# Kernel tuning notes

Measured on AMD Instinct MI355X. Metric: run time of the kernel, lower is better.

The kernel has to match this reference:

```python
import jax, jax.numpy as jnp
import numpy as np

DIM, DIN, NST, RK, K, BATCH, H, W = 64, 128, 16, 4, 4, 1, 128, 128


def conv2d(x, w, b=None, pad=0, groups=1):
    y = jax.lax.conv_general_dilated(x, w, (1, 1), [(pad, pad), (pad, pad)],
                                     dimension_numbers=('NCHW', 'OIHW', 'NCHW'),
                                     feature_group_count=groups)
    return y if b is None else y + b[None, :, None, None]


def layer_norm(x, g, b, eps=1e-5):
    mu = x.mean(-1, keepdims=True)
    var = x.var(-1, keepdims=True)
    return (x - mu) * jax.lax.rsqrt(var + eps) * g + b


def selective_scan(u, delta, A, Bs, Cs, D):
    # u, delta: (B,K,Din,L); A: (K,Din,N); Bs,Cs: (B,K,N,L); D: (K,Din)
    uT = jnp.moveaxis(u, -1, 0)
    dT = jnp.moveaxis(delta, -1, 0)
    BT = jnp.moveaxis(Bs, -1, 0)
    CT = jnp.moveaxis(Cs, -1, 0)
    h0 = jnp.zeros(u.shape[:3] + (A.shape[-1],), u.dtype)

    def step(h, inp):
        u_t, d_t, B_t, C_t = inp
        h = h * jnp.exp(d_t[..., None] * A) + (d_t * u_t)[..., None] * B_t[:, :, None, :]
        return h, jnp.einsum('bkdn,bkn->bkd', h, C_t)

    _, ys = jax.lax.scan(step, h0, (uT, dT, BT, CT))
    return jnp.moveaxis(ys, 0, -1) + u * D[None, :, :, None]


def ss2d(x, in_proj_w, conv_dw_w, conv_dw_b, x_proj_w, dt_w, dt_b, A_logs, Ds, on_g, on_b, out_w):
    # x: (B,H,W,C) -- VMamba-style SS2D with 4 scan directions
    Bb, Hh, Ww, C = x.shape
    L = Hh * Ww
    xz = jnp.einsum('bhwc,ec->bhwe', x, in_proj_w)
    xa, z = jnp.split(xz, 2, axis=-1)
    xa = jax.nn.silu(conv2d(xa.transpose(0, 3, 1, 2), conv_dw_w, conv_dw_b, pad=1, groups=DIN))
    x0 = xa.reshape(Bb, DIN, L)                          # row-major scan
    x1 = xa.transpose(0, 1, 3, 2).reshape(Bb, DIN, L)    # column-major scan
    xs = jnp.stack([x0, x1, jnp.flip(x0, -1), jnp.flip(x1, -1)], axis=1)  # (B,4,Din,L)
    x_dbl = jnp.einsum('bkdl,kcd->bkcl', xs, x_proj_w)
    dts, Bs, Cs = x_dbl[:, :, :RK], x_dbl[:, :, RK:RK + NST], x_dbl[:, :, RK + NST:]
    delta = jax.nn.softplus(jnp.einsum('bkrl,kdr->bkdl', dts, dt_w) + dt_b[None, :, :, None])
    ys = selective_scan(xs, delta, -jnp.exp(A_logs), Bs, Cs, Ds)  # (B,4,Din,L)

    def unwh(t):
        return t.reshape(Bb, DIN, Ww, Hh).transpose(0, 1, 3, 2).reshape(Bb, DIN, L)

    y = ys[:, 0] + jnp.flip(ys[:, 2], -1) + unwh(ys[:, 1]) + unwh(jnp.flip(ys[:, 3], -1))
    y = layer_norm(y.transpose(0, 2, 1).reshape(Bb, Hh, Ww, DIN), on_g, on_b)
    return jnp.einsum('bhwd,cd->bhwc', y * jax.nn.silu(z), out_w)


def setup_inputs():
    key = jax.random.key(0)
    ks = jax.random.split(key, 24)
    n = lambda k, s, sc=0.05: jax.random.normal(k, s, jnp.float32) * sc
    return dict(
        x=n(ks[0], (BATCH, DIM, H, W), 1.0),
        conv1_w=n(ks[1], (DIM, DIM, 3, 3)), conv1_b=n(ks[2], (DIM,)),
        conv2_w=n(ks[3], (DIM, DIM, 5, 5)), conv2_b=n(ks[4], (DIM,)),
        dw1a_w=n(ks[5], (2 * DIM, 2, 3, 3)), dw1a_b=n(ks[6], (2 * DIM,)),
        dw1b_w=n(ks[7], (DIM, 2 * DIM, 1, 1)), dw1b_b=n(ks[8], (DIM,)),
        dw2a_w=n(ks[9], (DIM, 1, 3, 3)), dw2a_b=n(ks[10], (DIM,)),
        dw2b_w=n(ks[11], (DIM, DIM, 1, 1)), dw2b_b=n(ks[12], (DIM,)),
        ln_g=jnp.ones((DIM,), jnp.float32), ln_b=jnp.zeros((DIM,), jnp.float32),
        in_proj_w=n(ks[13], (2 * DIN, DIM)),
        conv_dw_w=n(ks[14], (DIN, 1, 3, 3)), conv_dw_b=n(ks[15], (DIN,)),
        x_proj_w=n(ks[16], (K, RK + 2 * NST, DIN)),
        dt_w=n(ks[17], (K, DIN, RK)), dt_b=jnp.full((K, DIN), 0.01, jnp.float32),
        A_logs=jnp.tile(jnp.log(jnp.arange(1, NST + 1, dtype=jnp.float32)), (K, DIN, 1)),
        Ds=jnp.ones((K, DIN), jnp.float32),
        on_g=jnp.ones((DIN,), jnp.float32), on_b=jnp.zeros((DIN,), jnp.float32),
        out_w=n(ks[18], (DIM, DIN)),
    )


def reference(x, conv1_w, conv1_b, conv2_w, conv2_b, dw1a_w, dw1a_b, dw1b_w, dw1b_b,
              dw2a_w, dw2a_b, dw2b_w, dw2b_b, ln_g, ln_b, in_proj_w, conv_dw_w, conv_dw_b,
              x_proj_w, dt_w, dt_b, A_logs, Ds, on_g, on_b, out_w):
    res = x
    y = jax.nn.relu(jnp.concatenate([conv2d(x, conv1_w, conv1_b, pad=1),
                                     conv2d(x, conv2_w, conv2_b, pad=2)], axis=1))
    y = jax.nn.relu(conv2d(conv2d(y, dw1a_w, dw1a_b, pad=1, groups=DIM), dw1b_w, dw1b_b))
    # F.layer_norm over (C,H,W), no affine
    mu = y.mean((1, 2, 3), keepdims=True)
    var = y.var((1, 2, 3), keepdims=True)
    y = (y - mu) * jax.lax.rsqrt(var + 1e-5)
    # SS2D block: pre-LN + SS2D + residual, in NHWC
    yp = y.transpose(0, 2, 3, 1)
    yp = yp + ss2d(layer_norm(yp, ln_g, ln_b), in_proj_w, conv_dw_w, conv_dw_b,
                   x_proj_w, dt_w, dt_b, A_logs, Ds, on_g, on_b, out_w)
    y = yp.transpose(0, 3, 1, 2)
    y = jax.nn.relu(conv2d(conv2d(y, dw2a_w, dw2a_b, pad=1, groups=DIM), dw2b_w, dw2b_b))
    return y + res
```

## Files before the change

kernel.cpp:

```cpp
#include <hip/hip_runtime.h>

#define L 16384
#define NCH 128
#define CT  128

__device__ __forceinline__ float softplusf(float x){
  return (x > 20.f) ? x : log1pf(__expf(x));
}
__device__ __forceinline__ float siluf(float x){
  return x / (1.f + __expf(-x));
}
__device__ __forceinline__ float wave_sum(float v){
  #pragma unroll
  for (int o = 32; o; o >>= 1) v += __shfl_xor(v, o);
  return v;
}

__global__ __launch_bounds__(256) void k_prep(
    const float* __restrict__ w1, const float* __restrict__ w2,
    const float* __restrict__ ipw,
    float* __restrict__ wT1, float* __restrict__ wT2, float* __restrict__ ipwT)
{
  int g = blockIdx.x * 256 + threadIdx.x;
  if (g < 36864){
    int ci = g / 576, rem = g % 576, co = rem / 9, tap = rem % 9;
    wT1[g] = w1[(co*64 + ci)*9 + tap];
  } else if (g < 36864 + 102400){
    int g2 = g - 36864;
    int ci = g2 / 1600, rem = g2 % 1600, co = rem / 25, tap = rem % 25;
    wT2[g2] = w2[(co*64 + ci)*25 + tap];
  } else if (g < 36864 + 102400 + 16384){
    int g3 = g - 139264;
    int e = g3 & 255, c = g3 >> 8;
    ipwT[g3] = ipw[e*64 + c];
  }
}

template<int KS>
__global__ __launch_bounds__(256) void k_convC(
    const float* __restrict__ x, const float* __restrict__ wT,
    const float* __restrict__ b, float* __restrict__ y)
{
  constexpr int P = KS/2, NT = KS*KS;
  const int tid = threadIdx.x;
  const int col = tid & 127;
  const int rh  = tid >> 7;
  const int cg  = blockIdx.x & 15;
  const int rq  = blockIdx.x >> 4;
  const int r0  = rq*4 + rh*2;
  const int co0 = cg*4;
  float acc[2][4];
  #pragma unroll
  for (int a = 0; a < 4; ++a){ acc[0][a] = b[co0+a]; acc[1][a] = acc[0][a]; }

  for (int ci = 0; ci < 64; ++ci){
    const float* xp = x + ci*L;
    const float* wp = wT + (ci*64 + co0)*NT;
    #pragma unroll
    for (int ir = 0; ir < KS+1; ++ir){
      int gr = r0 - P + ir;
      float xrow[KS];
      if ((unsigned)gr < 128u){
        const float* xr = xp + gr*128;
        #pragma unroll
        for (int kx = 0; kx < KS; ++kx){
          int cc = col + kx - P;
          xrow[kx] = ((unsigned)cc < 128u) ? xr[cc] : 0.f;
        }
      } else {
        #pragma unroll
        for (int kx = 0; kx < KS; ++kx) xrow[kx] = 0.f;
      }
      #pragma unroll
      for (int q = 0; q < 2; ++q){
        int ky = ir - q;
        if (ky >= 0 && ky < KS){
          #pragma unroll
          for (int kx = 0; kx < KS; ++kx){
            #pragma unroll
            for (int a = 0; a < 4; ++a)
              acc[q][a] = fmaf(xrow[kx], wp[a*NT + ky*KS + kx], acc[q][a]);
          }
        }
      }
    }
  }
  #pragma unroll
  for (int q = 0; q < 2; ++q){
    const int p = (r0+q)*128 + col;
    #pragma unroll
    for (int a = 0; a < 4; ++a)
      y[(co0+a)*L + p] = fmaxf(acc[q][a], 0.f);
  }
}

__global__ __launch_bounds__(256) void k_dw1a(
    const float* __restrict__ y1, const float* __restrict__ w, const float* __restrict__ b,
    float* __restrict__ t1)
{
  int g = blockIdx.x * 256 + threadIdx.x;
  int p = g & (L-1);
  int o = g >> 14;
  int h = p >> 7, ww = p & 127;
  int grp = o >> 1;
  float acc = b[o];
  #pragma unroll
  for (int i = 0; i < 2; ++i){
    const float* xp = y1 + (grp*2 + i)*L;
    const float* wp = w + (o*2 + i)*9;
    #pragma unroll
    for (int ky = 0; ky < 3; ++ky){
      int hh = h + ky - 1;
      if ((unsigned)hh < 128u){
        #pragma unroll
        for (int kx = 0; kx < 3; ++kx){
          int wx = ww + kx - 1;
          if ((unsigned)wx < 128u)
            acc = fmaf(xp[hh*128 + wx], wp[ky*3+kx], acc);
        }
      }
    }
  }
  t1[o*L + p] = acc;
}

__global__ __launch_bounds__(256) void k_dw1b(
    const float* __restrict__ t1, const float* __restrict__ w, const float* __restrict__ b,
    float* __restrict__ y2, float* __restrict__ red)
{
  __shared__ float s[16][130];
  __shared__ float rs[4][2];
  int p0 = blockIdx.x * 16;
  for (int i = threadIdx.x; i < 2048; i += 256){
    int ci = i >> 4, dp = i & 15;
    s[dp][ci] = t1[ci*L + p0 + dp];
  }
  __syncthreads();
  int dp = threadIdx.x & 15, cg = threadIdx.x >> 4;
  float lsum = 0.f, lsq = 0.f;
  #pragma unroll
  for (int cc = 0; cc < 4; ++cc){
    int c = cg + cc*16;
    float acc = b[c];
    const float* wp = w + c*128;
    #pragma unroll 8
    for (int i = 0; i < 128; ++i) acc = fmaf(s[dp][i], wp[i], acc);
    acc = fmaxf(acc, 0.f);
    y2[c*L + p0 + dp] = acc;
    lsum += acc; lsq += acc*acc;
  }
  lsum = wave_sum(lsum); lsq = wave_sum(lsq);
  if ((threadIdx.x & 63) == 0){ rs[threadIdx.x>>6][0] = lsum; rs[threadIdx.x>>6][1] = lsq; }
  __syncthreads();
  if (threadIdx.x == 0){
    float a = rs[0][0]+rs[1][0]+rs[2][0]+rs[3][0];
    float q = rs[0][1]+rs[1][1]+rs[2][1]+rs[3][1];
    atomicAdd(&red[0], a);
    atomicAdd(&red[1], q);
  }
}

__global__ __launch_bounds__(256) void k_norm_inproj(
    const float* __restrict__ y2, const float* __restrict__ red,
    const float* __restrict__ ln_g, const float* __restrict__ ln_b,
    const float* __restrict__ ipwT,
    float* __restrict__ ynorm, float* __restrict__ xa_pre, float* __restrict__ sz)
{
  __shared__ float ws_s[16384];
  __shared__ float ls_s[64*33];
  __shared__ float mv_s[2][32];
  const int tid = threadIdx.x;
  const int p0 = blockIdx.x * 32;
  {
    const float4* src = (const float4*)ipwT;
    float4* dst = (float4*)ws_s;
    #pragma unroll
    for (int i = 0; i < 16; ++i) dst[tid + i*256] = src[tid + i*256];
  }
  const float invN = 1.f / 1048576.f;
  float mu = red[0] * invN;
  float var = red[1] * invN - mu*mu;
  float rsg = rsqrtf(var + 1e-5f);
  for (int i = tid; i < 2048; i += 256){
    int c = i >> 5, pix = i & 31;
    ls_s[c*33 + pix] = (y2[c*L + p0 + pix] - mu) * rsg;
  }
  __syncthreads();
  for (int i = tid; i < 2048; i += 256){
    int pix = i >> 6, c = i & 63;
    ynorm[(p0 + pix)*64 + c] = ls_s[c*33 + pix];
  }
  if (tid < 32){
    float s = 0.f, q = 0.f;
    #pragma unroll 8
    for (int c = 0; c < 64; ++c){
      float v = ls_s[c*33 + tid];
      s += v; q += v*v;
    }
    float m = s * (1.f/64.f);
    float va = q * (1.f/64.f) - m*m;
    mv_s[0][tid] = m;
    mv_s[1][tid] = rsqrtf(va + 1e-5f);
  }
  __syncthreads();
  for (int i = tid; i < 2048; i += 256){
    int c = i >> 5, pix = i & 31;
    float v = ls_s[c*33 + pix];
    ls_s[c*33 + pix] = (v - mv_s[0][pix]) * mv_s[1][pix] * ln_g[c] + ln_b[c];
  }
  __syncthreads();
  const int pix = tid & 31, eh = tid >> 5;
  float acc[32];
  #pragma unroll
  for (int j = 0; j < 32; ++j) acc[j] = 0.f;
  for (int c = 0; c < 64; ++c){
    float lnv = ls_s[c*33 + pix];
    const float4* w4 = (const float4*)(ws_s + c*256 + eh*32);
    #pragma unroll
    for (int j = 0; j < 8; ++j){
      float4 wq = w4[j];
      acc[j*4+0] = fmaf(lnv, wq.x, acc[j*4+0]);
      acc[j*4+1] = fmaf(lnv, wq.y, acc[j*4+1]);
      acc[j*4+2] = fmaf(lnv, wq.z, acc[j*4+2]);
      acc[j*4+3] = fmaf(lnv, wq.w, acc[j*4+3]);
    }
  }
  __syncthreads();
  float* szs = ws_s;
  const int p = p0 + pix;
  if (eh < 4){
    const int e0 = eh*32;
    #pragma unroll
    for (int j = 0; j < 32; ++j)
      xa_pre[(e0+j)*L + p] = acc[j];
  } else {
    const int j0 = (eh-4)*32;
    #pragma unroll
    for (int j = 0; j < 32; ++j)
      szs[pix*129 + j0 + j] = siluf(acc[j]);
  }
  __syncthreads();
  for (int i = tid; i < 32*128; i += 256){
    int pix2 = i >> 7, j = i & 127;
    sz[(p0 + pix2)*128 + j] = szs[pix2*129 + j];
  }
}

__global__ __launch_bounds__(256) void k_dwc(
    const float* __restrict__ xa, const float* __restrict__ w, const float* __restrict__ b,
    float* __restrict__ u)
{
  int g = blockIdx.x * 256 + threadIdx.x;
  int p = g & (L-1);
  int d = g >> 14;
  int h = p >> 7, ww = p & 127;
  const float* xp = xa + d*L;
  const float* wp = w + d*9;
  float acc = b[d];
  #pragma unroll
  for (int ky = 0; ky < 3; ++ky){
    int hh = h + ky - 1;
    if ((unsigned)hh < 128u){
      #pragma unroll
      for (int kx = 0; kx < 3; ++kx){
        int wx = ww + kx - 1;
        if ((unsigned)wx < 128u)
          acc = fmaf(xp[hh*128 + wx], wp[ky*3+kx], acc);
      }
    }
  }
  u[d*L + p] = siluf(acc);
}

template<int PASS>
__global__ __launch_bounds__(256) void k_proj(
    const float* __restrict__ u, const float* __restrict__ xw,
    const float* __restrict__ dtw, const float* __restrict__ dtb,
    float* __restrict__ delta_s, float* __restrict__ Bs, float* __restrict__ Cs,
    float* __restrict__ u_out)
{
  __shared__ float us[16][132];
  __shared__ float dts[16][2][4];
  int bb = blockIdx.x;
  int tid = threadIdx.x;
  for (int i = tid; i < 16*128; i += 256){
    int d = i >> 4, pix = i & 15;
    int idx = bb*16 + pix;
    int p;
    if (PASS == 0) p = idx;
    else           p = (idx & 127)*128 + (idx >> 7);
    us[pix][d] = u[d*L + p];
  }
  __syncthreads();
  for (int o = tid; o < 1152; o += 256){
    int pix = o / 72; int r = o % 72; int kk = r / 36; int c = r % 36;
    int k = (PASS == 0) ? kk*2 : kk*2 + 1;
    const float4* ur = (const float4*)(&us[pix][0]);
    const float4* wr = (const float4*)(xw + (k*36 + c)*128);
    float acc = 0.f;
    #pragma unroll
    for (int i = 0; i < 32; ++i){
      float4 a = ur[i], bw = wr[i];
      acc = fmaf(a.x, bw.x, acc); acc = fmaf(a.y, bw.y, acc);
      acc = fmaf(a.z, bw.z, acc); acc = fmaf(a.w, bw.w, acc);
    }
    int idx = bb*16 + pix;
    if (c < 4)        dts[pix][kk][c] = acc;
    else if (c < 20)  Bs[(k*L + idx)*16 + (c-4)]  = acc;
    else              Cs[(k*L + idx)*16 + (c-20)] = acc;
  }
  __syncthreads();
  int d = tid & 127, ph = tid >> 7;
  #pragma unroll
  for (int pp = 0; pp < 8; ++pp){
    int pix = pp*2 + ph;
    int idx = bb*16 + pix;
    #pragma unroll
    for (int kk = 0; kk < 2; ++kk){
      int k = (PASS == 0) ? kk*2 : kk*2 + 1;
      const float4 dw = *((const float4*)(dtw + (k*128 + d)*4));
      float acc = dtb[k*128 + d];
      acc = fmaf(dts[pix][kk][0], dw.x, acc);
      acc = fmaf(dts[pix][kk][1], dw.y, acc);
      acc = fmaf(dts[pix][kk][2], dw.z, acc);
      acc = fmaf(dts[pix][kk][3], dw.w, acc);
      delta_s[(k*L + idx)*128 + d] = softplusf(acc);
    }
    u_out[idx*128 + d] = us[pix][d];
  }
}

__global__ __launch_bounds__(256) void k_scan1(
    const float* __restrict__ delta_s, const float* __restrict__ u_row,
    const float* __restrict__ u_col, const float* __restrict__ Bs,
    const float* __restrict__ Alog, float* __restrict__ P, float* __restrict__ S)
{
  int blk = blockIdx.x;
  int k = blk >> 7, ch = blk & (NCH-1);
  int tid = threadIdx.x;
  int d = tid & 127, nh = tid >> 7;
  const float* u_s = (k & 1) ? u_col : u_row;
  float A[8], Pv[8], Sv[8];
  #pragma unroll
  for (int j = 0; j < 8; ++j){
    A[j] = -__expf(Alog[(k*128 + d)*16 + nh*8 + j]);
    Pv[j] = 1.f; Sv[j] = 0.f;
  }
  int base = ch*CT;
  for (int t = 0; t < CT; ++t){
    int tl = base + t;
    int pos = (k < 2) ? tl : (L-1 - tl);
    float dl = delta_s[(k*L + pos)*128 + d];
    float du = dl * u_s[pos*128 + d];
    const float* Br = Bs + (k*L + pos)*16 + nh*8;
    #pragma unroll
    for (int j = 0; j < 8; ++j){
      float a = __expf(dl * A[j]);
      Sv[j] = fmaf(Sv[j], a, du * Br[j]);
      Pv[j] *= a;
    }
  }
  #pragma unroll
  for (int j = 0; j < 8; ++j){
    int o = (blk*16 + nh*8 + j)*128 + d;
    P[o] = Pv[j]; S[o] = Sv[j];
  }
}

__global__ __launch_bounds__(256) void k_scan2(
    const float* __restrict__ P, const float* __restrict__ S, float* __restrict__ hst)
{
  int g = blockIdx.x * 256 + threadIdx.x;
  int d = g & 127, n = (g >> 7) & 15, k = g >> 11;
  float h = 0.f;
  for (int c = 0; c < NCH; ++c){
    int o = (((k*NCH + c)*16) + n)*128 + d;
    hst[o] = h;
    h = fmaf(P[o], h, S[o]);
  }
}

__global__ __launch_bounds__(256) void k_scan3(
    const float* __restrict__ delta_s, const float* __restrict__ u_row,
    const float* __restrict__ u_col, const float* __restrict__ Bs,
    const float* __restrict__ Cs, const float* __restrict__ Alog,
    const float* __restrict__ hst, float* __restrict__ ys)
{
  int blk = blockIdx.x;
  int k = blk >> 7, ch = blk & (NCH-1);
  int tid = threadIdx.x;
  int d = tid >> 1, nh = tid & 1;
  const float* u_s = (k & 1) ? u_col : u_row;
  float A[8], h[8];
  #pragma unroll
  for (int j = 0; j < 8; ++j){
    A[j] = -__expf(Alog[(k*128 + d)*16 + nh*8 + j]);
    h[j] = hst[(blk*16 + nh*8 + j)*128 + d];
  }
  int base = ch*CT;
  for (int t = 0; t < CT; ++t){
    int tl = base + t;
    int pos = (k < 2) ? tl : (L-1 - tl);
    float dl = delta_s[(k*L + pos)*128 + d];
    float du = dl * u_s[pos*128 + d];
    const float* Br = Bs + (k*L + pos)*16 + nh*8;
    const float* Cr = Cs + (k*L + pos)*16 + nh*8;
    float y = 0.f;
    #pragma unroll
    for (int j = 0; j < 8; ++j){
      float a = __expf(dl * A[j]);
      h[j] = fmaf(h[j], a, du * Br[j]);
      y = fmaf(h[j], Cr[j], y);
    }
    y += __shfl_xor(y, 1);
    if (nh == 0) ys[(k*L + pos)*128 + d] = y;
  }
}

__global__ __launch_bounds__(128) void k_combine(
    const float* __restrict__ ys, const float* __restrict__ u_row,
    const float* __restrict__ Ds, const float* __restrict__ on_g,
    const float* __restrict__ on_b, const float* __restrict__ sz,
    const float* __restrict__ out_w, const float* __restrict__ ynorm,
    float* __restrict__ yp2)
{
  __shared__ float gs[128];
  __shared__ float rbuf[2][2];
  int p = blockIdx.x;
  int d = threadIdx.x;
  int h = p >> 7, w = p & 127;
  int pT = w*128 + h;
  float y = ys[(0*L + p )*128 + d] + ys[(2*L + p )*128 + d]
          + ys[(1*L + pT)*128 + d] + ys[(3*L + pT)*128 + d];
  float sumD = Ds[d] + Ds[128 + d] + Ds[256 + d] + Ds[384 + d];
  y = fmaf(u_row[p*128 + d], sumD, y);
  float s = wave_sum(y);
  float sq = wave_sum(y*y);
  if ((d & 63) == 0){ rbuf[d>>6][0] = s; rbuf[d>>6][1] = sq; }
  __syncthreads();
  float ts = rbuf[0][0] + rbuf[1][0];
  float tq = rbuf[0][1] + rbuf[1][1];
  float m = ts * (1.f/128.f);
  float va = tq * (1.f/128.f) - m*m;
  float yn = (y - m) * rsqrtf(va + 1e-5f) * on_g[d] + on_b[d];
  gs[d] = yn * sz[p*128 + d];
  __syncthreads();
  if (d < 64){
    const float4* wr = (const float4*)(out_w + d*128);
    const float4* gr = (const float4*)gs;
    float acc = 0.f;
    #pragma unroll
    for (int i = 0; i < 32; ++i){
      float4 a = gr[i], bw = wr[i];
      acc = fmaf(a.x, bw.x, acc); acc = fmaf(a.y, bw.y, acc);
      acc = fmaf(a.z, bw.z, acc); acc = fmaf(a.w, bw.w, acc);
    }
    yp2[p*64 + d] = ynorm[p*64 + d] + acc;
  }
}

__global__ __launch_bounds__(256) void k_dw2a(
    const float* __restrict__ yp2, const float* __restrict__ w,
    const float* __restrict__ b, float* __restrict__ t2)
{
  int g = blockIdx.x * 256 + threadIdx.x;
  int c = g & 63;
  int p = g >> 6;
  int h = p >> 7, ww = p & 127;
  const float* wp = w + c*9;
  float acc = b[c];
  #pragma unroll
  for (int ky = 0; ky < 3; ++ky){
    int hh = h + ky - 1;
    if ((unsigned)hh < 128u){
      #pragma unroll
      for (int kx = 0; kx < 3; ++kx){
        int wx = ww + kx - 1;
        if ((unsigned)wx < 128u)
          acc = fmaf(yp2[(hh*128 + wx)*64 + c], wp[ky*3+kx], acc);
      }
    }
  }
  t2[p*64 + c] = acc;
}

__global__ __launch_bounds__(256) void k_dw2b(
    const float* __restrict__ t2, const float* __restrict__ w,
    const float* __restrict__ b, const float* __restrict__ x,
    float* __restrict__ out)
{
  __shared__ float s[16][65];
  int p0 = blockIdx.x * 16;
  for (int i = threadIdx.x; i < 1024; i += 256){
    int pix = i >> 6, c = i & 63;
    s[pix][c] = t2[(p0 + pix)*64 + c];
  }
  __syncthreads();
  int dp = threadIdx.x & 15, cg = threadIdx.x >> 4;
  #pragma unroll
  for (int cc = 0; cc < 4; ++cc){
    int c = cg + cc*16;
    float acc = b[c];
    const float* wp = w + c*64;
    #pragma unroll 8
    for (int i = 0; i < 64; ++i) acc = fmaf(s[dp][i], wp[i], acc);
    acc = fmaxf(acc, 0.f);
    int p = p0 + dp;
    out[c*L + p] = acc + x[c*L + p];
  }
}

extern "C" void kernel_launch(void* const* d_in, const int* in_sizes, int n_in,
                              void* d_out, int out_size, void* d_ws, size_t ws_size,
                              hipStream_t stream)
{
  const float* x       = (const float*)d_in[0];
  const float* conv1_w = (const float*)d_in[1];
  const float* conv1_b = (const float*)d_in[2];
  const float* conv2_w = (const float*)d_in[3];
  const float* conv2_b = (const float*)d_in[4];
  const float* dw1a_w  = (const float*)d_in[5];
  const float* dw1a_b  = (const float*)d_in[6];
  const float* dw1b_w  = (const float*)d_in[7];
  const float* dw1b_b  = (const float*)d_in[8];
  const float* dw2a_w  = (const float*)d_in[9];
  const float* dw2a_b  = (const float*)d_in[10];
  const float* dw2b_w  = (const float*)d_in[11];
  const float* dw2b_b  = (const float*)d_in[12];
  const float* ln_g    = (const float*)d_in[13];
  const float* ln_b    = (const float*)d_in[14];
  const float* ipw     = (const float*)d_in[15];
  const float* cdw_w   = (const float*)d_in[16];
  const float* cdw_b   = (const float*)d_in[17];
  const float* xw      = (const float*)d_in[18];
  const float* dtw     = (const float*)d_in[19];
  const float* dtb     = (const float*)d_in[20];
  const float* Alog    = (const float*)d_in[21];
  const float* DsArr   = (const float*)d_in[22];
  const float* on_g    = (const float*)d_in[23];
  const float* on_b    = (const float*)d_in[24];
  const float* out_w   = (const float*)d_in[25];
  float* out = (float*)d_out;

  char* ws = (char*)d_ws;
  const size_t MB = 1048576ull;
  float* y1      = (float*)(ws + 0*MB);
  float* t1      = (float*)(ws + 8*MB);
  float* y2      = (float*)(ws + 16*MB);
  float* xa_pre  = (float*)(ws + 20*MB);
  float* wT1     = (float*)(ws + 28*MB);
  float* wT2     = (float*)(ws + 28*MB + 524288);
  float* ipwT    = (float*)(ws + 29*MB);
  float* red     = (float*)(ws + 30*MB);
  float* ysb     = (float*)(ws + 0*MB);
  float* delta_s = (float*)(ws + 32*MB);
  float* ynorm   = (float*)(ws + 64*MB);
  float* sz      = (float*)(ws + 68*MB);
  float* u       = (float*)(ws + 76*MB);
  float* u_row   = (float*)(ws + 84*MB);
  float* u_col   = (float*)(ws + 92*MB);
  float* Bsb     = (float*)(ws + 100*MB);
  float* Csb     = (float*)(ws + 104*MB);
  float* Pb      = (float*)(ws + 108*MB);
  float* Sb      = (float*)(ws + 112*MB);
  float* hst     = (float*)(ws + 116*MB);
  float* yp2     = (float*)(ws + 108*MB);
  float* t2      = (float*)(ws + 112*MB);

  hipMemsetAsync(red, 0, 2*sizeof(float), stream);

  k_prep    <<<608, 256, 0, stream>>>(conv1_w, conv2_w, ipw, wT1, wT2, ipwT);
  k_convC<3><<<512, 256, 0, stream>>>(x, wT1, conv1_b, y1);
  k_convC<5><<<512, 256, 0, stream>>>(x, wT2, conv2_b, y1 + 64*L);
  k_dw1a  <<<8192, 256, 0, stream>>>(y1, dw1a_w, dw1a_b, t1);
  k_dw1b  <<<1024, 256, 0, stream>>>(t1, dw1b_w, dw1b_b, y2, red);
  k_norm_inproj<<<512, 256, 0, stream>>>(y2, red, ln_g, ln_b, ipwT, ynorm, xa_pre, sz);
  k_dwc   <<<8192, 256, 0, stream>>>(xa_pre, cdw_w, cdw_b, u);
  k_proj<0><<<1024, 256, 0, stream>>>(u, xw, dtw, dtb, delta_s, Bsb, Csb, u_row);
  k_proj<1><<<1024, 256, 0, stream>>>(u, xw, dtw, dtb, delta_s, Bsb, Csb, u_col);
  k_scan1 <<<4*NCH, 256, 0, stream>>>(delta_s, u_row, u_col, Bsb, Alog, Pb, Sb);
  k_scan2 <<<32, 256, 0, stream>>>(Pb, Sb, hst);
  k_scan3 <<<4*NCH, 256, 0, stream>>>(delta_s, u_row, u_col, Bsb, Csb, Alog, hst, ysb);
  k_combine<<<16384, 128, 0, stream>>>(ysb, u_row, DsArr, on_g, on_b, sz, out_w, ynorm, yp2);
  k_dw2a  <<<4096, 256, 0, stream>>>(yp2, dw2a_w, dw2a_b, t2);
  k_dw2b  <<<1024, 256, 0, stream>>>(t2, dw2b_w, dw2b_b, x, out);
}
```

Measured before the change: 745.7 us.

## Split dense convs over input channels with zero-padded input and reduction pass

The input is first copied into a zero-padded buffer so the 3x3 and 5x5 convolution inner loops can drop their bounds checks. Each conv is then split four ways over input channels, raising the block count from 512 to 2048 per conv, and each split writes partial sums. A new reduction kernel adds the partials, the bias and the ReLU. The aim is better occupancy and lighter inner loops, paid for with extra partial-sum traffic (about 32 MB written and read back) and two extra launches.

```diff
diff --git a/kernel.cpp b/kernel.cpp
--- a/kernel.cpp
+++ b/kernel.cpp
@@ -3,6 +3,8 @@
 #define L 16384
 #define NCH 128
 #define CT  128
+#define PH 132
+#define PW 136
 
 __device__ __forceinline__ float softplusf(float x){
   return (x > 20.f) ? x : log1pf(__expf(x));
@@ -36,41 +38,50 @@
   }
 }
 
+__global__ __launch_bounds__(256) void k_pad(
+    const float* __restrict__ x, float* __restrict__ xpad)
+{
+  int g = blockIdx.x * 256 + threadIdx.x;
+  int ci = g / (PH*PW);
+  int r  = (g / PW) % PH;
+  int c  = g % PW;
+  float v = 0.f;
+  int ur = r - 2, uc = c - 2;
+  if ((unsigned)ur < 128u && (unsigned)uc < 128u)
+    v = x[ci*L + ur*128 + uc];
+  xpad[g] = v;
+}
+
 template<int KS>
-__global__ __launch_bounds__(256) void k_convC(
-    const float* __restrict__ x, const float* __restrict__ wT,
-    const float* __restrict__ b, float* __restrict__ y)
+__global__ __launch_bounds__(256) void k_convD(
+    const float* __restrict__ xpad, const float* __restrict__ wT,
+    float* __restrict__ part)
 {
   constexpr int P = KS/2, NT = KS*KS;
   const int tid = threadIdx.x;
   const int col = tid & 127;
   const int rh  = tid >> 7;
-  const int cg  = blockIdx.x & 15;
-  const int rq  = blockIdx.x >> 4;
+  const int b   = blockIdx.x;
+  const int cg  = b & 15;
+  const int rq  = (b >> 4) & 31;
+  const int s   = b >> 9;
   const int r0  = rq*4 + rh*2;
   const int co0 = cg*4;
   float acc[2][4];
   #pragma unroll
-  for (int a = 0; a < 4; ++a){ acc[0][a] = b[co0+a]; acc[1][a] = acc[0][a]; }
-
-  for (int ci = 0; ci < 64; ++ci){
-    const float* xp = x + ci*L;
+  for (int q = 0; q < 2; ++q)
+    #pragma unroll
+    for (int a = 0; a < 4; ++a) acc[q][a] = 0.f;
+
+  const int ci0 = s*16;
+  for (int ci = ci0; ci < ci0+16; ++ci){
+    const float* xb = xpad + ci*(PH*PW) + (r0 - P + 2)*PW + (col - P + 2);
     const float* wp = wT + (ci*64 + co0)*NT;
     #pragma unroll
     for (int ir = 0; ir < KS+1; ++ir){
-      int gr = r0 - P + ir;
       float xrow[KS];
-      if ((unsigned)gr < 128u){
-        const float* xr = xp + gr*128;
-        #pragma unroll
-        for (int kx = 0; kx < KS; ++kx){
-          int cc = col + kx - P;
-          xrow[kx] = ((unsigned)cc < 128u) ? xr[cc] : 0.f;
-        }
-      } else {
-        #pragma unroll
-        for (int kx = 0; kx < KS; ++kx) xrow[kx] = 0.f;
-      }
+      #pragma unroll
+      for (int kx = 0; kx < KS; ++kx) xrow[kx] = xb[ir*PW + kx];
       #pragma unroll
       for (int q = 0; q < 2; ++q){
         int ky = ir - q;
@@ -90,8 +101,29 @@
     const int p = (r0+q)*128 + col;
     #pragma unroll
     for (int a = 0; a < 4; ++a)
-      y[(co0+a)*L + p] = fmaxf(acc[q][a], 0.f);
-  }
+      part[(s*64 + co0+a)*L + p] = acc[q][a];
+  }
+}
+
+__global__ __launch_bounds__(256) void k_convred(
+    const float* __restrict__ part1, const float* __restrict__ part2,
+    const float* __restrict__ b1, const float* __restrict__ b2,
+    float* __restrict__ y1)
+{
+  int g = blockIdx.x * 256 + threadIdx.x;
+  int ch = g >> 14, p = g & (L-1);
+  float v;
+  if (ch < 64){
+    v = b1[ch];
+    #pragma unroll
+    for (int s = 0; s < 4; ++s) v += part1[(s*64 + ch)*L + p];
+  } else {
+    int c = ch - 64;
+    v = b2[c];
+    #pragma unroll
+    for (int s = 0; s < 4; ++s) v += part2[(s*64 + c)*L + p];
+  }
+  y1[ch*L + p] = fmaxf(v, 0.f);
 }
 
 __global__ __launch_bounds__(256) void k_dw1a(
@@ -547,11 +579,14 @@
   float* y1      = (float*)(ws + 0*MB);
   float* t1      = (float*)(ws + 8*MB);
   float* y2      = (float*)(ws + 16*MB);
+  float* xpad    = (float*)(ws + 20*MB);
   float* xa_pre  = (float*)(ws + 20*MB);
   float* wT1     = (float*)(ws + 28*MB);
   float* wT2     = (float*)(ws + 28*MB + 524288);
   float* ipwT    = (float*)(ws + 29*MB);
   float* red     = (float*)(ws + 30*MB);
+  float* part1   = (float*)(ws + 32*MB);
+  float* part2   = (float*)(ws + 48*MB);
   float* ysb     = (float*)(ws + 0*MB);
   float* delta_s = (float*)(ws + 32*MB);
   float* ynorm   = (float*)(ws + 64*MB);
@@ -570,8 +605,10 @@
   hipMemsetAsync(red, 0, 2*sizeof(float), stream);
 
   k_prep    <<<608, 256, 0, stream>>>(conv1_w, conv2_w, ipw, wT1, wT2, ipwT);
-  k_convC<3><<<512, 256, 0, stream>>>(x, wT1, conv1_b, y1);
-  k_convC<5><<<512, 256, 0, stream>>>(x, wT2, conv2_b, y1 + 64*L);
+  k_pad     <<<4488, 256, 0, stream>>>(x, xpad);
+  k_convD<3><<<2048, 256, 0, stream>>>(xpad, wT1, part1);
+  k_convD<5><<<2048, 256, 0, stream>>>(xpad, wT2, part2);
+  k_convred <<<8192, 256, 0, stream>>>(part1, part2, conv1_b, conv2_b, y1);
   k_dw1a  <<<8192, 256, 0, stream>>>(y1, dw1a_w, dw1a_b, t1);
   k_dw1b  <<<1024, 256, 0, stream>>>(t1, dw1b_w, dw1b_b, y2, red);
   k_norm_inproj<<<512, 256, 0, stream>>>(y2, red, ln_g, ln_b, ipwT, ynorm, xa_pre, sz);
```

Measured after the change: 636.4 us. 14.7% less time.
